# Kernel tuning notes

Measured on AMD Instinct MI355X. Metric: run time of the kernel, lower is better.

## Reference

```python
import jax, jax.numpy as jnp
import numpy as np

B, Z, A, H = 2048, 64, 8, 512

def setup_inputs() -> dict:
    key = jax.random.key(0)
    ks = jax.random.split(key, 7)
    s = 1.0 / np.sqrt(H).astype(np.float32)
    z = jax.random.normal(ks[0], (B, Z), jnp.float32)
    # PyTorch LSTM params, gate order [i, f, g, o]
    W_ih = jax.random.uniform(ks[1], (4 * H, A + Z), jnp.float32, -s, s)
    W_hh = jax.random.uniform(ks[2], (4 * H, H), jnp.float32, -s, s)
    b_ih = jax.random.uniform(ks[3], (4 * H,), jnp.float32, -s, s)
    b_hh = jax.random.uniform(ks[4], (4 * H,), jnp.float32, -s, s)
    W_out = jax.random.uniform(ks[5], (A, H), jnp.float32, -s, s)
    b_out = jax.random.uniform(ks[6], (A,), jnp.float32, -s, s)
    return {"z": z, "W_ih": W_ih, "W_hh": W_hh, "b_ih": b_ih, "b_hh": b_hh,
            "W_out": W_out, "b_out": b_out, "seq_len": 64}


def reference(z, W_ih, W_hh, b_ih, b_hh, W_out, b_out, seq_len):
    batch = z.shape[0]
    hidden = W_hh.shape[1]
    act = W_out.shape[0]
    # dec_in_t = [zeros_a, z] is identical at every timestep -> hoist input proj
    dec_in = jnp.concatenate([jnp.zeros((batch, act), z.dtype), z], axis=-1)
    x_proj = dec_in @ W_ih.T + b_ih + b_hh  # (B, 4H), constant per step

    def step(carry, _):
        h, c = carry
        gates = x_proj + h @ W_hh.T  # (B, 4H)
        i, f, g, o = jnp.split(gates, 4, axis=-1)
        i = jax.nn.sigmoid(i)
        f = jax.nn.sigmoid(f)
        g = jnp.tanh(g)
        o = jax.nn.sigmoid(o)
        c = f * c + i * g
        h = o * jnp.tanh(c)
        return (h, c), h

    init = (jnp.zeros((batch, hidden), z.dtype), jnp.zeros((batch, hidden), z.dtype))
    _, hs = jax.lax.scan(step, init, None, length=seq_len)  # (T, B, H)
    hs = jnp.transpose(hs, (1, 0, 2))  # (B, T, H)
    return hs @ W_out.T + b_out  # (B, T, A)
```

## Files before the change

kernel.cpp:

```cpp
#include <hip/hip_runtime.h>


#define HID   512
#define TSTEP 64
#define KCAT  576

typedef unsigned long long u64;
typedef __attribute__((ext_vector_type(8))) short bf16x8;
typedef __attribute__((ext_vector_type(4))) float f32x4;

__device__ inline unsigned short f2bf(float f) {
  unsigned int u = __builtin_bit_cast(unsigned int, f);
  unsigned int r = (u + 0x7fffu + ((u >> 16) & 1u)) >> 16;
  return (unsigned short)r;
}
__device__ inline float sigm(float x) { return 1.0f / (1.0f + __expf(-x)); }
__device__ inline float tanh_f(float x) { return 1.0f - 2.0f / (__expf(2.0f * x) + 1.0f); }

__device__ inline void gl16(const unsigned short* g, unsigned short* l) {
  __builtin_amdgcn_global_load_lds(
      (const __attribute__((address_space(1))) unsigned int*)g,
      (__attribute__((address_space(3))) unsigned int*)l, 16, 0, 0);
}
__device__ inline void ldc16(bf16x8& d, const unsigned short* p) {
  asm volatile("global_load_dwordx4 %0, %1, off sc0 sc1"
               : "=v"(d) : "v"(p) : "memory");
}

#define ATOMLD(PTR) __hip_atomic_load((PTR), __ATOMIC_RELAXED, __HIP_MEMORY_SCOPE_AGENT)
#define ATOMST(PTR, V) __hip_atomic_store((PTR), (V), __ATOMIC_RELAXED, __HIP_MEMORY_SCOPE_AGENT)
#define WAITV(N) do { asm volatile("s_waitcnt vmcnt(" #N ")" ::: "memory"); \
                      __builtin_amdgcn_sched_barrier(0); } while (0)

__global__ void k_prep(const float* __restrict__ z, const float* __restrict__ wih,
                       const float* __restrict__ whh, const float* __restrict__ bih,
                       const float* __restrict__ bhh,
                       unsigned short* __restrict__ wcat, unsigned short* __restrict__ zbf,
                       float* __restrict__ bias) {
  int c = blockIdx.x * 256 + threadIdx.x;
  if (c < 147456) {
    int n = c / 72, kc = (c % 72) * 8;
    unsigned short u[8];
#pragma unroll
    for (int e = 0; e < 8; ++e) {
      int k = kc + e;
      float v = (k < 512) ? whh[(size_t)n * 512 + k] : wih[(size_t)n * 72 + 8 + (k - 512)];
      u[e] = f2bf(v);
    }
    *(bf16x8*)&wcat[(size_t)n * KCAT + kc] = *(bf16x8*)u;
  } else if (c < 163840) {
    int i = c - 147456;
    int row = i >> 3, kc = (i & 7) * 8;
    unsigned short u[8];
#pragma unroll
    for (int e = 0; e < 8; ++e) u[e] = f2bf(z[(size_t)row * 64 + kc + e]);
    *(bf16x8*)&zbf[(size_t)row * 64 + kc] = *(bf16x8*)u;
  } else if (c < 165888) {
    int n = c - 163840;
    bias[n] = bih[n] + bhh[n];
  }
}

__global__ void k_zero(int* __restrict__ flags) {
  int g = blockIdx.x * 256 + threadIdx.x;
  if (g < TSTEP * 512) flags[g] = 0;
}

struct P {
  const unsigned short *wcat, *zbf;
  const float *bias, *wout, *bout;
  unsigned short *h0, *h1;
  float* out;
  int* flags;
};

#define SMEM_SZ 70656

__global__ __launch_bounds__(256, 2) void k_persist(P p) {
  extern __shared__ char smem[];
  unsigned short* Bb[3] = {(unsigned short*)smem, (unsigned short*)(smem + 16384),
                           (unsigned short*)(smem + 32768)};
  unsigned short* wo = (unsigned short*)(smem + 49152);
  unsigned short* hO = (unsigned short*)(smem + 65536);

  const int bid = blockIdx.x;
  const int nt = bid >> 5, bt = bid & 31;
  const int tid = threadIdx.x;
  const int lane = tid & 63;
  const int wv = tid >> 6;
  const int mq = wv >> 1, nh = wv & 1;
  const int cl = lane & 15, q8 = lane >> 4;
  const int b0 = bt * 64, j0 = nt * 32;

  const int rS = tid >> 3;
  const int xS = ((tid & 7) ^ (rS & 7)) * 8;
  const unsigned short* srcB[4];
#pragma unroll
  for (int k = 0; k < 4; ++k) {
    int rB = k * 32 + rS;
    int n = (rB >> 5) * HID + j0 + (rB & 31);
    srcB[k] = p.wcat + (size_t)n * KCAT + xS;
  }
#define STAGEB(BUF, CHUNK) { _Pragma("unroll") for (int k4 = 0; k4 < 4; ++k4) \
    gl16(srcB[k4] + (CHUNK) * 64, &Bb[BUF][(k4 * 256 + wv * 64) * 8]); }

  if (nt == 0) {
    int r = tid >> 4, s0 = tid & 15;
#pragma unroll
    for (int i = 0; i < 4; ++i) {
      int s = s0 + i * 16;
      unsigned short u[8] = {0, 0, 0, 0, 0, 0, 0, 0};
      if (r < 8) {
        const float* wp = p.wout + (size_t)r * 512 + s * 8;
        float4 f0 = *(const float4*)wp;
        float4 f1 = *(const float4*)(wp + 4);
        u[0] = f2bf(f0.x); u[1] = f2bf(f0.y); u[2] = f2bf(f0.z); u[3] = f2bf(f0.w);
        u[4] = f2bf(f1.x); u[5] = f2bf(f1.y); u[6] = f2bf(f1.z); u[7] = f2bf(f1.w);
      }
      int off = r * 512 + (s >> 3) * 64 + (((s & 7) ^ (r & 7)) * 8);
      *(bf16x8*)&wo[off] = *(bf16x8*)u;
    }
  }
  bf16x8 azr[4];
#pragma unroll
  for (int m = 0; m < 2; ++m)
#pragma unroll
    for (int ks = 0; ks < 2; ++ks)
      azr[m * 2 + ks] = *(const bf16x8*)&p.zbf[(size_t)(b0 + mq * 32 + m * 16 + cl) * 64 + ks * 32 + q8 * 8];

  float bias_r[4];
#pragma unroll
  for (int g = 0; g < 4; ++g) bias_r[g] = p.bias[g * HID + j0 + nh * 16 + cl];
  f32x4 c0 = {0, 0, 0, 0}, c1 = {0, 0, 0, 0};
  f32x4 acc[4][2];
  f32x4 accp0, accp1;
  const float boutv = (cl < 8) ? p.bout[cl] : 0.0f;
  const int arow = tid >> 2, aseg = tid & 3;
  const int r0 = b0 + mq * 32 + cl;

  bf16x8 ra[3][4];
  auto issueA = [&](bf16x8 d[4], const unsigned short* hp, int kk) {
    const unsigned short* base0 = hp + (size_t)r0 * HID + kk * 64 + q8 * 8;
    const unsigned short* base1 = base0 + 16 * HID;
    ldc16(d[0], base0);
    ldc16(d[1], base0 + 32);
    ldc16(d[2], base1);
    ldc16(d[3], base1 + 32);
  };

  auto gate_mfma = [&](const bf16x8 a4[4], const unsigned short* Bl, int kkv) {
    __builtin_amdgcn_s_setprio(1);
#pragma unroll
    for (int ks = 0; ks < 2; ++ks) {
      const int sx = ((ks * 4 + q8) ^ (cl & 7)) * 8;
      bf16x8 af0 = a4[ks], af1 = a4[2 + ks];
#pragma unroll
      for (int g = 0; g < 4; ++g) {
        bf16x8 bf = *(const bf16x8*)&Bl[(g * 32 + nh * 16 + cl) * 64 + sx];
        acc[g][0] = __builtin_amdgcn_mfma_f32_16x16x32_bf16(af0, bf, acc[g][0], 0, 0, 0);
        acc[g][1] = __builtin_amdgcn_mfma_f32_16x16x32_bf16(af1, bf, acc[g][1], 0, 0, 0);
      }
      if (nt == 0 && nh == 0 && kkv < 8) {
        bf16x8 wf = *(const bf16x8*)&wo[cl * 512 + kkv * 64 + sx];
        accp0 = __builtin_amdgcn_mfma_f32_16x16x32_bf16(af0, wf, accp0, 0, 0, 0);
        accp1 = __builtin_amdgcn_mfma_f32_16x16x32_bf16(af1, wf, accp1, 0, 0, 0);
      }
    }
    __builtin_amdgcn_s_setprio(0);
  };

  auto cell_store_flag = [&](unsigned short* hcur, int t) {
#pragma unroll
    for (int fm = 0; fm < 2; ++fm) {
      f32x4 cold = fm ? c1 : c0;
      f32x4 cn;
#pragma unroll
      for (int r = 0; r < 4; ++r) {
        float iv = sigm(acc[0][fm][r]);
        float fv = sigm(acc[1][fm][r]);
        float gv = tanh_f(acc[2][fm][r]);
        float ov = sigm(acc[3][fm][r]);
        float cv = fv * cold[r] + iv * gv;
        cn[r] = cv;
        hO[(mq * 32 + fm * 16 + q8 * 4 + r) * 40 + nh * 16 + cl] = f2bf(ov * tanh_f(cv));
      }
      if (fm) c1 = cn; else c0 = cn;
    }
    __syncthreads();
    u64 u0 = *(const u64*)&hO[arow * 40 + aseg * 8];
    u64 u1 = *(const u64*)&hO[arow * 40 + aseg * 8 + 4];
    u64* dst = (u64*)(hcur + (size_t)(b0 + arow) * HID + j0 + aseg * 8);
    ATOMST(dst, u0);
    ATOMST(dst + 1, u1);
    STAGEB(0, 0);
    STAGEB(1, 1);
    WAITV(8);
    __builtin_amdgcn_s_barrier();
    if (tid == 0)
      ATOMST(&p.flags[t * 512 + bt * 16 + nt], 1);
  };

#define SPIN(T) do { \
    if (tid < 16) { \
      const int* fp = &p.flags[(T) * 512 + bt * 16 + tid]; \
      while (ATOMLD(fp) == 0) __builtin_amdgcn_s_sleep(1); \
    } \
    __syncthreads(); } while (0)

  STAGEB(2, 8);
  asm volatile("s_waitcnt vmcnt(0) lgkmcnt(0)" ::: "memory");
  __builtin_amdgcn_sched_barrier(0);
  __builtin_amdgcn_s_barrier();
#pragma unroll
  for (int g = 0; g < 4; ++g) {
    f32x4 v = {bias_r[g], bias_r[g], bias_r[g], bias_r[g]};
    acc[g][0] = v; acc[g][1] = v;
  }
  gate_mfma(azr, Bb[2], 8);
  cell_store_flag(p.h0, 0);

  for (int t = 1; t < TSTEP; ++t) {
    const unsigned short* hprev = (t & 1) ? p.h0 : p.h1;
    unsigned short* hcur = (t & 1) ? p.h1 : p.h0;
    SPIN(t - 1);

    issueA(ra[0], hprev, 0);
    issueA(ra[1], hprev, 1);
    issueA(ra[2], hprev, 2);
    WAITV(8);
    __builtin_amdgcn_s_barrier();

#pragma unroll
    for (int g = 0; g < 4; ++g) {
      f32x4 v = {bias_r[g], bias_r[g], bias_r[g], bias_r[g]};
      acc[g][0] = v; acc[g][1] = v;
    }
    { f32x4 v = {boutv, boutv, boutv, boutv}; accp0 = v; accp1 = v; }

#pragma unroll
    for (int kk = 0; kk <= 8; ++kk) {
      gate_mfma(kk < 8 ? ra[kk % 3] : azr, Bb[kk % 3], kk);
      if (kk == 8) break;
      if (kk <= 4) issueA(ra[kk % 3], hprev, kk + 3);
      if (kk <= 6) STAGEB((kk + 2) % 3, kk + 2);
      if (kk == 0)      WAITV(12);
      else if (kk <= 4) WAITV(8);
      else if (kk <= 6) WAITV(4);
      else              WAITV(0);
      __builtin_amdgcn_s_barrier();
    }

    if (nt == 0 && nh == 0 && cl < 8) {
      const int tt = t - 1;
#pragma unroll
      for (int r = 0; r < 4; ++r) {
        int b = b0 + mq * 32 + q8 * 4 + r;
        p.out[((size_t)b * 64 + tt) * 8 + cl] = accp0[r];
        p.out[((size_t)(b + 16) * 64 + tt) * 8 + cl] = accp1[r];
      }
    }
    cell_store_flag(hcur, t);
  }

  if (nt == 0) {
    SPIN(63);
    const unsigned short* h63 = p.h1;
    issueA(ra[0], h63, 0);
    issueA(ra[1], h63, 1);
    issueA(ra[2], h63, 2);
    f32x4 ap0 = {boutv, boutv, boutv, boutv};
    f32x4 ap1 = ap0;
#pragma unroll
    for (int kk = 0; kk < 8; ++kk) {
      if (kk <= 5)      WAITV(8);
      else if (kk == 6) WAITV(4);
      else              WAITV(0);
      if (nh == 0) {
#pragma unroll
        for (int ks = 0; ks < 2; ++ks) {
          const int sx = ((ks * 4 + q8) ^ (cl & 7)) * 8;
          bf16x8 wf = *(const bf16x8*)&wo[cl * 512 + kk * 64 + sx];
          ap0 = __builtin_amdgcn_mfma_f32_16x16x32_bf16(ra[kk % 3][ks], wf, ap0, 0, 0, 0);
          ap1 = __builtin_amdgcn_mfma_f32_16x16x32_bf16(ra[kk % 3][2 + ks], wf, ap1, 0, 0, 0);
        }
      }
      if (kk <= 4) issueA(ra[kk % 3], h63, kk + 3);
    }
    if (nh == 0 && cl < 8) {
#pragma unroll
      for (int r = 0; r < 4; ++r) {
        int b = b0 + mq * 32 + q8 * 4 + r;
        p.out[((size_t)b * 64 + 63) * 8 + cl] = ap0[r];
        p.out[((size_t)(b + 16) * 64 + 63) * 8 + cl] = ap1[r];
      }
    }
  }
#undef STAGEB
#undef SPIN
}

template <int GATES, int PROJ>
__global__ __launch_bounds__(256, 2) void k_stepF(
    const unsigned short* __restrict__ hprev, unsigned short* __restrict__ hnext,
    const unsigned short* __restrict__ wcat, const unsigned short* __restrict__ zbf,
    const float* __restrict__ wout, const float* __restrict__ bias,
    const float* __restrict__ bout, float* __restrict__ cst,
    float* __restrict__ out, int t) {
  __shared__ unsigned short Ab[2][64 * 64];
  __shared__ unsigned short Bb[2][128 * 64];
  __shared__ unsigned short wo_lds[16 * 512];
  __shared__ unsigned short hO[64 * 40];

  const int bid = blockIdx.x;
  const int nt = GATES ? (((bid & 7) << 1) | ((bid >> 8) & 1)) : 0;
  const int bt = GATES ? ((bid >> 3) & 31) : bid;
  const int tid = threadIdx.x;
  const int lane = tid & 63;
  const int wv = tid >> 6;
  const int mq = wv >> 1, nh = wv & 1;
  const int cl = lane & 15, q8 = lane >> 4;
  const int b0 = bt * 64, j0 = nt * 32;

  const int rA = tid >> 3;
  const int xA = ((tid & 7) ^ (rA & 7)) * 8;
  const unsigned short* srcA0 = hprev + (size_t)(b0 + rA) * HID + xA;
  const unsigned short* srcA1 = hprev + (size_t)(b0 + 32 + rA) * HID + xA;
  const unsigned short* srcZ0 = zbf + (size_t)(b0 + rA) * 64 + xA;
  const unsigned short* srcZ1 = zbf + (size_t)(b0 + 32 + rA) * 64 + xA;
  const unsigned short* srcB[4];
#pragma unroll
  for (int k = 0; k < 4; ++k) {
    int rB = k * 32 + rA;
    int n = (rB >> 5) * HID + j0 + (rB & 31);
    srcB[k] = wcat + (size_t)n * KCAT + xA;
  }

  auto do_stage = [&](int buf, int kkv) {
    if (GATES) {
      if (kkv == 8) {
        gl16(srcZ0, &Ab[buf][(wv * 64) * 8]);
        gl16(srcZ1, &Ab[buf][(256 + wv * 64) * 8]);
      } else {
        gl16(srcA0 + kkv * 64, &Ab[buf][(wv * 64) * 8]);
        gl16(srcA1 + kkv * 64, &Ab[buf][(256 + wv * 64) * 8]);
      }
#pragma unroll
      for (int k = 0; k < 4; ++k)
        gl16(srcB[k] + kkv * 64, &Bb[buf][(k * 256 + wv * 64) * 8]);
    } else {
      gl16(srcA0 + kkv * 64, &Ab[buf][(wv * 64) * 8]);
      gl16(srcA1 + kkv * 64, &Ab[buf][(256 + wv * 64) * 8]);
    }
  };

  if (PROJ) {
    int r = tid >> 4, s0 = tid & 15;
#pragma unroll
    for (int i = 0; i < 4; ++i) {
      int s = s0 + i * 16;
      unsigned short u[8] = {0, 0, 0, 0, 0, 0, 0, 0};
      if (r < 8) {
        const float* wp = wout + (size_t)r * 512 + s * 8;
        float4 f0 = *(const float4*)wp;
        float4 f1 = *(const float4*)(wp + 4);
        u[0] = f2bf(f0.x); u[1] = f2bf(f0.y); u[2] = f2bf(f0.z); u[3] = f2bf(f0.w);
        u[4] = f2bf(f1.x); u[5] = f2bf(f1.y); u[6] = f2bf(f1.z); u[7] = f2bf(f1.w);
      }
      int off = r * 512 + (s >> 3) * 64 + (((s & 7) ^ (r & 7)) * 8);
      *(bf16x8*)&wo_lds[off] = *(bf16x8*)u;
    }
  }

  f32x4 acc[4][2];
  if (GATES) {
#pragma unroll
    for (int g = 0; g < 4; ++g) {
      float bv = bias[g * HID + j0 + nh * 16 + cl];
      f32x4 v = {bv, bv, bv, bv};
      acc[g][0] = v; acc[g][1] = v;
    }
  }
  f32x4 accp0 = {0, 0, 0, 0}, accp1 = {0, 0, 0, 0};
  if (PROJ) {
    float bo = (cl < 8) ? bout[cl] : 0.0f;
    f32x4 v = {bo, bo, bo, bo};
    accp0 = v; accp1 = v;
  }

  const size_t cbase = ((size_t)bid * 256 + tid) * 8;
  f32x4 c0 = {0, 0, 0, 0}, c1 = {0, 0, 0, 0};
  if (GATES && t > 0) { c0 = *(const f32x4*)&cst[cbase]; c1 = *(const f32x4*)&cst[cbase + 4]; }

  auto mfma_block = [&](int bu, int kkv) {
    const unsigned short* Al = Ab[bu];
    const unsigned short* Bl = Bb[bu];
#pragma unroll
    for (int ks = 0; ks < 2; ++ks) {
      const int sx = ((ks * 4 + q8) ^ (cl & 7)) * 8;
      bf16x8 af0 = *(const bf16x8*)&Al[(mq * 32 + cl) * 64 + sx];
      bf16x8 af1 = *(const bf16x8*)&Al[(mq * 32 + 16 + cl) * 64 + sx];
      if (GATES) {
#pragma unroll
        for (int g = 0; g < 4; ++g) {
          bf16x8 bf = *(const bf16x8*)&Bl[(g * 32 + nh * 16 + cl) * 64 + sx];
          acc[g][0] = __builtin_amdgcn_mfma_f32_16x16x32_bf16(af0, bf, acc[g][0], 0, 0, 0);
          acc[g][1] = __builtin_amdgcn_mfma_f32_16x16x32_bf16(af1, bf, acc[g][1], 0, 0, 0);
        }
      }
      if (PROJ && nh == 0 && kkv < 8) {
        bf16x8 wf = *(const bf16x8*)&wo_lds[cl * 512 + kkv * 64 + sx];
        accp0 = __builtin_amdgcn_mfma_f32_16x16x32_bf16(af0, wf, accp0, 0, 0, 0);
        accp1 = __builtin_amdgcn_mfma_f32_16x16x32_bf16(af1, wf, accp1, 0, 0, 0);
      }
    }
  };

  if (GATES && t == 0) {
    do_stage(0, 8);
    asm volatile("s_waitcnt vmcnt(0) lgkmcnt(0)" ::: "memory");
    __builtin_amdgcn_s_barrier();
    mfma_block(0, 8);
  } else {
    do_stage(0, 0);
    do_stage(1, 1);
    if (GATES) asm volatile("s_waitcnt vmcnt(6) lgkmcnt(0)" ::: "memory");
    else       asm volatile("s_waitcnt vmcnt(2) lgkmcnt(0)" ::: "memory");
    __builtin_amdgcn_s_barrier();
    const int kkEnd = GATES ? 8 : 7;
    for (int kk = 0;; ++kk) {
      mfma_block(kk & 1, kk);
      if (kk == kkEnd) break;
      asm volatile("" ::: "memory");
      __builtin_amdgcn_s_barrier();
      if (kk + 2 <= kkEnd) {
        do_stage(kk & 1, kk + 2);
        if (GATES) asm volatile("s_waitcnt vmcnt(6)" ::: "memory");
        else       asm volatile("s_waitcnt vmcnt(2)" ::: "memory");
      } else {
        asm volatile("s_waitcnt vmcnt(0)" ::: "memory");
      }
      asm volatile("" ::: "memory");
      __builtin_amdgcn_s_barrier();
    }
  }

  if (PROJ && nh == 0 && cl < 8) {
    const int tt = t - 1;
#pragma unroll
    for (int r = 0; r < 4; ++r) {
      int b = b0 + mq * 32 + q8 * 4 + r;
      out[((size_t)b * 64 + tt) * 8 + cl] = accp0[r];
      out[((size_t)(b + 16) * 64 + tt) * 8 + cl] = accp1[r];
    }
  }

  if (GATES) {
#pragma unroll
    for (int fm = 0; fm < 2; ++fm) {
      f32x4 cold = fm ? c1 : c0;
      f32x4 cn;
#pragma unroll
      for (int r = 0; r < 4; ++r) {
        float iv = sigm(acc[0][fm][r]);
        float fv = sigm(acc[1][fm][r]);
        float gv = tanh_f(acc[2][fm][r]);
        float ov = sigm(acc[3][fm][r]);
        float cv = fv * cold[r] + iv * gv;
        cn[r] = cv;
        hO[(mq * 32 + fm * 16 + q8 * 4 + r) * 40 + nh * 16 + cl] = f2bf(ov * tanh_f(cv));
      }
      if (fm) c1 = cn; else c0 = cn;
    }
    *(f32x4*)&cst[cbase] = c0;
    *(f32x4*)&cst[cbase + 4] = c1;
    __syncthreads();
    int row = tid >> 2, sg4 = tid & 3;
    unsigned short tmp[8];
#pragma unroll
    for (int e = 0; e < 8; ++e) tmp[e] = hO[row * 40 + sg4 * 8 + e];
    *(int4*)&hnext[(size_t)(b0 + row) * HID + j0 + sg4 * 8] = *(int4*)tmp;
  }
}

extern "C" void kernel_launch(void* const* d_in, const int* in_sizes, int n_in,
                              void* d_out, int out_size, void* d_ws, size_t ws_size,
                              hipStream_t stream) {
  const float* z    = (const float*)d_in[0];
  const float* wih  = (const float*)d_in[1];
  const float* whh  = (const float*)d_in[2];
  const float* bih  = (const float*)d_in[3];
  const float* bhh  = (const float*)d_in[4];
  const float* wout = (const float*)d_in[5];
  const float* bout = (const float*)d_in[6];
  float* out = (float*)d_out;

  char* ws = (char*)d_ws;
  unsigned short* wcat = (unsigned short*)(ws);
  unsigned short* zbf  = (unsigned short*)(ws + 2359296);
  float* bias          = (float*)(ws + 2621440);
  unsigned short* h0   = (unsigned short*)(ws + 2629632);
  unsigned short* h1   = (unsigned short*)(ws + 4726784);
  int* flags           = (int*)(ws + 6823936);
  float* cst           = (float*)(ws + 6955008);

  k_prep<<<dim3(648), dim3(256), 0, stream>>>(z, wih, whh, bih, bhh, wcat, zbf, bias);
  k_zero<<<dim3(128), dim3(256), 0, stream>>>(flags);

  P pp;
  pp.wcat = wcat; pp.zbf = zbf; pp.bias = bias; pp.wout = wout; pp.bout = bout;
  pp.h0 = h0; pp.h1 = h1; pp.out = out; pp.flags = flags;

  hipFuncSetAttribute((const void*)k_persist,
                      hipFuncAttributeMaxDynamicSharedMemorySize, SMEM_SZ);
  void* args[] = {&pp};
  hipError_t e = hipLaunchCooperativeKernel((const void*)k_persist, dim3(512), dim3(256),
                                            args, SMEM_SZ, stream);
  if (e == hipSuccess) return;

  for (int t = 0; t < TSTEP; ++t) {
    const unsigned short* hp = (t & 1) ? h0 : h1;
    unsigned short* hn = (t & 1) ? h1 : h0;
    if (t == 0)
      k_stepF<1, 0><<<dim3(512), dim3(256), 0, stream>>>(hp, hn, wcat, zbf, wout, bias,
                                                         bout, cst, out, t);
    else
      k_stepF<1, 1><<<dim3(512), dim3(256), 0, stream>>>(hp, hn, wcat, zbf, wout, bias,
                                                         bout, cst, out, t);
  }
  k_stepF<0, 1><<<dim3(32), dim3(256), 0, stream>>>(h1, h0, wcat, zbf, wout, bias,
                                                    bout, cst, out, TSTEP);
}
```

Measured before the change: 911.7 us.

## Wait only on needed h chunks and rotate K order per block

Each block now begins its K loop at a different chunk of the previous hidden state (offset by its column tile). It spins only on the flags for the first four chunks it needs, then checks the remaining flags one chunk at a time inside the K loop, instead of waiting for all 16 producer blocks up front. The aim is to overlap the per-step grid-wide wait with useful MFMA work and to spread the load across memory. In exchange it adds more spin checks inside the inner loop and makes the correctness of the memory ordering more delicate.

```diff
diff --git a/kernel.cpp b/kernel.cpp
--- a/kernel.cpp
+++ b/kernel.cpp
@@ -91,6 +91,7 @@
   const int mq = wv >> 1, nh = wv & 1;
   const int cl = lane & 15, q8 = lane >> 4;
   const int b0 = bt * 64, j0 = nt * 32;
+  const int c0 = nt >> 1;
 
   const int rS = tid >> 3;
   const int xS = ((tid & 7) ^ (rS & 7)) * 8;
@@ -131,7 +132,7 @@
   float bias_r[4];
 #pragma unroll
   for (int g = 0; g < 4; ++g) bias_r[g] = p.bias[g * HID + j0 + nh * 16 + cl];
-  f32x4 c0 = {0, 0, 0, 0}, c1 = {0, 0, 0, 0};
+  f32x4 c0v = {0, 0, 0, 0}, c1v = {0, 0, 0, 0};
   f32x4 acc[4][2];
   f32x4 accp0, accp1;
   const float boutv = (cl < 8) ? p.bout[cl] : 0.0f;
@@ -172,7 +173,7 @@
   auto cell_store_flag = [&](unsigned short* hcur, int t) {
 #pragma unroll
     for (int fm = 0; fm < 2; ++fm) {
-      f32x4 cold = fm ? c1 : c0;
+      f32x4 cold = fm ? c1v : c0v;
       f32x4 cn;
 #pragma unroll
       for (int r = 0; r < 4; ++r) {
@@ -184,7 +185,7 @@
         cn[r] = cv;
         hO[(mq * 32 + fm * 16 + q8 * 4 + r) * 40 + nh * 16 + cl] = f2bf(ov * tanh_f(cv));
       }
-      if (fm) c1 = cn; else c0 = cn;
+      if (fm) c1v = cn; else c0v = cn;
     }
     __syncthreads();
     u64 u0 = *(const u64*)&hO[arow * 40 + aseg * 8];
@@ -192,21 +193,14 @@
     u64* dst = (u64*)(hcur + (size_t)(b0 + arow) * HID + j0 + aseg * 8);
     ATOMST(dst, u0);
     ATOMST(dst + 1, u1);
-    STAGEB(0, 0);
-    STAGEB(1, 1);
+    STAGEB(0, c0);
+    STAGEB(1, (c0 + 1) & 7);
     WAITV(8);
     __builtin_amdgcn_s_barrier();
     if (tid == 0)
       ATOMST(&p.flags[t * 512 + bt * 16 + nt], 1);
   };
 
-#define SPIN(T) do { \
-    if (tid < 16) { \
-      const int* fp = &p.flags[(T) * 512 + bt * 16 + tid]; \
-      while (ATOMLD(fp) == 0) __builtin_amdgcn_s_sleep(1); \
-    } \
-    __syncthreads(); } while (0)
-
   STAGEB(2, 8);
   asm volatile("s_waitcnt vmcnt(0) lgkmcnt(0)" ::: "memory");
   __builtin_amdgcn_sched_barrier(0);
@@ -222,11 +216,18 @@
   for (int t = 1; t < TSTEP; ++t) {
     const unsigned short* hprev = (t & 1) ? p.h0 : p.h1;
     unsigned short* hcur = (t & 1) ? p.h1 : p.h0;
-    SPIN(t - 1);
-
-    issueA(ra[0], hprev, 0);
-    issueA(ra[1], hprev, 1);
-    issueA(ra[2], hprev, 2);
+    const int* fbase = &p.flags[(t - 1) * 512 + bt * 16];
+
+    if (tid < 8) {
+      int rcq = (c0 + (tid >> 1)) & 7;
+      const int* fp = fbase + rcq * 2 + (tid & 1);
+      while (ATOMLD(fp) == 0) __builtin_amdgcn_s_sleep(1);
+    }
+    __syncthreads();
+
+    issueA(ra[0], hprev, c0);
+    issueA(ra[1], hprev, (c0 + 1) & 7);
+    issueA(ra[2], hprev, (c0 + 2) & 7);
     WAITV(8);
     __builtin_amdgcn_s_barrier();
 
@@ -238,15 +239,20 @@
     { f32x4 v = {boutv, boutv, boutv, boutv}; accp0 = v; accp1 = v; }
 
 #pragma unroll
-    for (int kk = 0; kk <= 8; ++kk) {
-      gate_mfma(kk < 8 ? ra[kk % 3] : azr, Bb[kk % 3], kk);
-      if (kk == 8) break;
-      if (kk <= 4) issueA(ra[kk % 3], hprev, kk + 3);
-      if (kk <= 6) STAGEB((kk + 2) % 3, kk + 2);
-      if (kk == 0)      WAITV(12);
-      else if (kk <= 4) WAITV(8);
-      else if (kk <= 6) WAITV(4);
-      else              WAITV(0);
+    for (int j = 0; j <= 8; ++j) {
+      const int rcj = (c0 + j) & 7;
+      gate_mfma(j < 8 ? ra[j % 3] : azr, Bb[j % 3], j < 8 ? rcj : 8);
+      if (j == 8) break;
+      if (j <= 4) issueA(ra[j % 3], hprev, (c0 + j + 3) & 7);
+      if (j <= 6) STAGEB((j + 2) % 3, (j + 2 < 8) ? ((c0 + j + 2) & 7) : 8);
+      if (j <= 3 && tid < 2) {
+        const int* fp = fbase + ((c0 + j + 4) & 7) * 2 + tid;
+        while (ATOMLD(fp) == 0) __builtin_amdgcn_s_sleep(1);
+      }
+      if (j == 0)      WAITV(12);
+      else if (j <= 4) WAITV(8);
+      else if (j <= 6) WAITV(4);
+      else             WAITV(0);
       __builtin_amdgcn_s_barrier();
     }
 
@@ -263,7 +269,11 @@
   }
 
   if (nt == 0) {
-    SPIN(63);
+    if (tid < 16) {
+      const int* fp = &p.flags[63 * 512 + bt * 16 + tid];
+      while (ATOMLD(fp) == 0) __builtin_amdgcn_s_sleep(1);
+    }
+    __syncthreads();
     const unsigned short* h63 = p.h1;
     issueA(ra[0], h63, 0);
     issueA(ra[1], h63, 1);
@@ -296,7 +306,6 @@
     }
   }
 #undef STAGEB
-#undef SPIN
 }
 
 template <int GATES, int PROJ>
```

After: 901.2 us. Within noise of the previous version (-1.1%).
